# Kernel optimization log

Measured on AMD Instinct MI355X. Metric: run time of the kernel, lower is better.

The kernel has to match this reference:

```python
import jax, jax.numpy as jnp
import numpy as np

PATCH = 3
PAD = 1  # (patchsize-1)//2
PRETRAIN_DIM = 1024
TARGET_DIM = 1024
OUT_H, OUT_W = 224, 224


def _pool_matrix(L_in, L_out):
    """Matrix P s.t. x @ P == torch.adaptive_avg_pool1d(x, L_out)."""
    P = np.zeros((L_in, L_out), dtype=np.float32)
    for i in range(L_out):
        s = (i * L_in) // L_out
        e = -((-(i + 1) * L_in) // L_out)  # ceil
        P[s:e, i] = 1.0 / (e - s)
    return jnp.asarray(P)


def patchify(x):
    """[B,C,H,W] -> [B,H*W,C,3,3], matching Unfold(k=3,s=1,p=1) + reshape/permute."""
    B, C, H, W = x.shape
    xp = jnp.pad(x, ((0, 0), (0, 0), (PAD, PAD), (PAD, PAD)))
    # [B,C,3,3,H,W] with kernel offsets (ki,kj)
    cols = jnp.stack([
        jnp.stack([xp[:, :, i:i + H, j:j + W] for j in range(PATCH)], axis=3)
        for i in range(PATCH)], axis=2)
    return cols.transpose(0, 4, 5, 1, 2, 3).reshape(B, H * W, C, PATCH, PATCH)


def resize_bilinear(x, oh, ow):
    """Bilinear resize of last two dims, align_corners=False (torch semantics)."""
    H, W = x.shape[-2], x.shape[-1]

    def idx(L, O):
        src = (jnp.arange(O, dtype=jnp.float32) + 0.5) * (L / O) - 0.5
        src = jnp.clip(src, 0.0, L - 1)
        i0 = jnp.floor(src).astype(jnp.int32)
        i1 = jnp.minimum(i0 + 1, L - 1)
        return i0, i1, src - i0

    r0, r1, wr = idx(H, oh)
    c0, c1, wc = idx(W, ow)
    xr = x[..., r0, :] * (1.0 - wr)[:, None] + x[..., r1, :] * wr[:, None]
    return xr[..., c0] * (1.0 - wc) + xr[..., c1] * wc


def setup_inputs() -> dict:
    key = jax.random.key(0)
    k1, k2, k3 = jax.random.split(key, 3)
    return {
        "feat1": jax.random.normal(k1, (8, 512, 28, 28), dtype=jnp.float32),
        "feat2": jax.random.normal(k2, (8, 1024, 14, 14), dtype=jnp.float32),
        "memory": jax.random.normal(k3, (20000, 1024), dtype=jnp.float32),
    }


def reference(feat1, feat2, memory):
    B, C1, H1, W1 = feat1.shape
    _, C2, H2, W2 = feat2.shape
    N = H1 * W1  # reference patch grid

    # --- patchify (Unfold k=3 s=1 p=1) ---
    p1 = patchify(feat1)                      # [B, N, C1, 3, 3]
    p2 = patchify(feat2)                      # [B, H2*W2, C2, 3, 3]

    # --- multiscale bilinear resize of layer-2 patch grid to ref grid ---
    g = p2.reshape(B, H2, W2, C2, PATCH, PATCH).transpose(0, 3, 4, 5, 1, 2)  # [B,C2,3,3,H2,W2]
    g = resize_bilinear(g, H1, W1)                                           # [B,C2,3,3,H1,W1]
    p2 = g.transpose(0, 4, 5, 1, 2, 3).reshape(B, N, C2, PATCH, PATCH)

    # --- Preprocessing: adaptive_avg_pool1d over flattened patch -> pretrain dim ---
    f1 = p1.reshape(B * N, C1 * PATCH * PATCH) @ _pool_matrix(C1 * PATCH * PATCH, PRETRAIN_DIM)
    f2 = p2.reshape(B * N, C2 * PATCH * PATCH) @ _pool_matrix(C2 * PATCH * PATCH, PRETRAIN_DIM)

    # --- Aggregator: stack layers, adaptive pool to target dim ---
    stacked = jnp.stack([f1, f2], axis=1).reshape(B * N, 2 * PRETRAIN_DIM)
    feats = stacked @ _pool_matrix(2 * PRETRAIN_DIM, TARGET_DIM)  # [B*N, D]

    # --- kNN memory-bank scoring (k=1): min Euclidean distance ---
    d2 = (jnp.sum(feats * feats, axis=-1, keepdims=True)
          - 2.0 * feats @ memory.T
          + jnp.sum(memory * memory, axis=-1))  # [B*N, M]
    dist = jnp.sqrt(jnp.maximum(d2, 0.0))
    patch_scores = jnp.min(dist, axis=1)       # [B*N]

    # --- unpatch + score + raw segmentation map ---
    ps = patch_scores.reshape(B, N)
    image_scores = jnp.max(ps, axis=1)                           # [B]
    raw_maps = resize_bilinear(ps.reshape(B, H1, W1), OUT_H, OUT_W)  # [B,224,224]
    return image_scores, raw_maps
```

## Files before the change

kernel.cpp:

```cpp
#include <hip/hip_runtime.h>
#include <hip/hip_bf16.h>
#include <math.h>

#define BQ 8
#define C1N 512
#define N1 784
#define C2N 1024
#define M2 196
#define NROWS 6272
#define MEMN 20000
#define MEMNP 20096
#define DIMK 1024
#define NKB 32
#define KTB 4096
#define OUTHW 50176
#define NTILEA 49
#define NTILEB 157
#define NWG (NTILEB * NTILEA)

typedef unsigned char u8;
typedef long long i64v;

typedef __attribute__((ext_vector_type(4))) float f32x4;

static __device__ __forceinline__ unsigned int f2ord(float f) {
  unsigned int b = __float_as_uint(f);
  return (b & 0x80000000u) ? ~b : (b | 0x80000000u);
}
static __device__ __forceinline__ float ord2f(unsigned int u) {
  unsigned int b = (u & 0x80000000u) ? (u ^ 0x80000000u) : ~u;
  return __uint_as_float(b);
}

static __device__ __forceinline__ int pack4_fp8(float a, float b, float c, float d) {
  int lo = __builtin_amdgcn_cvt_pk_fp8_f32(a, b, 0, false);
  return __builtin_amdgcn_cvt_pk_fp8_f32(c, d, lo, true);
}
static __device__ __forceinline__ float sumsq4_fp8(int w) {
  float f0 = __builtin_amdgcn_cvt_f32_fp8(w, 0);
  float f1 = __builtin_amdgcn_cvt_f32_fp8(w, 1);
  float f2 = __builtin_amdgcn_cvt_f32_fp8(w, 2);
  float f3 = __builtin_amdgcn_cvt_f32_fp8(w, 3);
  return f0 * f0 + f1 * f1 + f2 * f2 + f3 * f3;
}

static __device__ __forceinline__ void gload16(const void* g, void* l) {
  __builtin_amdgcn_global_load_lds((const __attribute__((address_space(1))) void*)g,
                                   (__attribute__((address_space(3))) void*)l, 16, 0, 0);
}

static __device__ __forceinline__ size_t tiled_idx(int grow, int k) {
  int tile = grow >> 7, row = grow & 127;
  int kb = k >> 5, c = (k >> 3) & 3, e = k & 7;
  return (((size_t)(tile * NKB + kb) * 4 + c) * 128 + row) * 8 + e;
}

static __device__ __forceinline__ float f1val(const float* __restrict__ x, int b, unsigned L) {
  unsigned h = L % 28u; unsigned t = L / 28u;
  unsigned ki = t % 3u; t /= 3u;
  unsigned c = t % 512u; t /= 512u;
  unsigned w = t % 28u; unsigned kj = t / 28u;
  unsigned y = h + ki - 1u;
  unsigned xx = w + kj - 1u;
  if (y >= 28u || xx >= 28u) return 0.f;
  return x[(((size_t)b * 512u + c) * 28u + y) * 28u + xx];
}
static __device__ __forceinline__ float f2val(const float* __restrict__ x, int b, unsigned L) {
  unsigned h = L % 14u; unsigned t = L / 14u;
  unsigned ki = t % 3u; t /= 3u;
  unsigned c = t % 1024u; t /= 1024u;
  unsigned w = t % 14u; unsigned kj = t / 14u;
  unsigned y = h + ki - 1u;
  unsigned xx = w + kj - 1u;
  if (y >= 14u || xx >= 14u) return 0.f;
  return x[(((size_t)b * 1024u + c) * 14u + y) * 14u + xx];
}

__global__ __launch_bounds__(256) void feat_a_fp8(const float* __restrict__ feat1,
                                                  u8* __restrict__ At) {
  int id = blockIdx.x * 256 + threadIdx.x;
  if (id >= BQ * 64 * N1) return;
  int n = id % N1; int t = id / N1;
  int jc = t % 64; int b = t / 64;
  float v[8];
#pragma unroll
  for (int e = 0; e < 8; ++e) {
    int j = jc * 8 + e;
    unsigned L0 = 9u * (unsigned)(512 * n + j);
    float s = 0.f;
#pragma unroll
    for (int u = 0; u < 9; ++u) s += f1val(feat1, b, L0 + u);
    s += f1val(feat1, b, L0 + 4u);
    v[e] = s * 0.1f;
  }
  int w0 = pack4_fp8(v[0], v[1], v[2], v[3]);
  int w1 = pack4_fp8(v[4], v[5], v[6], v[7]);
  *(int2*)&At[tiled_idx(b * N1 + n, jc * 8)] = make_int2(w0, w1);
}

__global__ __launch_bounds__(256) void feat_b_stage1(const float* __restrict__ feat2,
                                                     float* __restrict__ H2all) {
  int b = blockIdx.x / M2;
  int n2 = blockIdx.x % M2;
  for (int i = threadIdx.x; i < 512; i += 256) {
    unsigned L0 = 18u * (unsigned)(512 * n2 + i);
    float s = 0.f;
#pragma unroll
    for (int u = 0; u < 18; ++u) s += f2val(feat2, b, L0 + u);
    H2all[((size_t)b * M2 + n2) * 512 + i] = s * (1.0f / 18.0f);
  }
}

__global__ __launch_bounds__(256) void feat_b_stage2_fp8(const float* __restrict__ H2all,
                                                         u8* __restrict__ At) {
  int id = blockIdx.x * 256 + threadIdx.x;
  if (id >= BQ * 64 * N1) return;
  int n = id % N1; int t = id / N1;
  int ic = t % 64; int b = t / 64;
  int y = n / 28, x = n % 28;
  float sy = 0.5f * (float)y - 0.25f;
  sy = fminf(fmaxf(sy, 0.f), 13.f);
  int y0 = (int)sy, y1 = min(y0 + 1, 13);
  float wy = sy - (float)y0;
  float sx = 0.5f * (float)x - 0.25f;
  sx = fminf(fmaxf(sx, 0.f), 13.f);
  int x0 = (int)sx, x1 = min(x0 + 1, 13);
  float wx = sx - (float)x0;
  float w00 = (1.f - wy) * (1.f - wx), w10 = wy * (1.f - wx);
  float w01 = (1.f - wy) * wx, w11 = wy * wx;
  const float* h00 = H2all + ((size_t)b * M2 + y0 * 14 + x0) * 512 + ic * 8;
  const float* h10 = H2all + ((size_t)b * M2 + y1 * 14 + x0) * 512 + ic * 8;
  const float* h01 = H2all + ((size_t)b * M2 + y0 * 14 + x1) * 512 + ic * 8;
  const float* h11 = H2all + ((size_t)b * M2 + y1 * 14 + x1) * 512 + ic * 8;
  float v[8];
#pragma unroll
  for (int e = 0; e < 8; ++e)
    v[e] = w00 * h00[e] + w10 * h10[e] + w01 * h01[e] + w11 * h11[e];
  int w0 = pack4_fp8(v[0], v[1], v[2], v[3]);
  int w1 = pack4_fp8(v[4], v[5], v[6], v[7]);
  *(int2*)&At[tiled_idx(b * N1 + n, 512 + ic * 8)] = make_int2(w0, w1);
}

__global__ __launch_bounds__(256) void memconv_fp8(const float* __restrict__ mem,
                                                   u8* __restrict__ Bt) {
  int gid = blockIdx.x * 256 + threadIdx.x;
  if (gid >= NTILEB * NKB * 512) return;
  int tile = gid >> 14;
  int within = gid & 16383;
  int kb = within >> 9;
  int u = within & 511;
  int c = u >> 7, row = u & 127;
  int n = tile * 128 + row;
  int k0 = kb * 32 + c * 8;
  int w0 = 0, w1 = 0;
  if (n < MEMN) {
    const float* src = mem + (size_t)n * DIMK + k0;
    float4 a = *(const float4*)src;
    float4 b = *(const float4*)(src + 4);
    w0 = pack4_fp8(a.x, a.y, a.z, a.w);
    w1 = pack4_fp8(b.x, b.y, b.z, b.w);
  }
  *(int2*)&Bt[(size_t)gid * 8] = make_int2(w0, w1);
}

__global__ __launch_bounds__(256) void fnorm_fp8(const u8* __restrict__ At,
                                                 float* __restrict__ fnorm) {
  int row = blockIdx.x * 4 + (threadIdx.x >> 6);
  int lane = threadIdx.x & 63;
  float s = 0.f;
#pragma unroll
  for (int qq = 0; qq < 2; ++qq) {
    int kc = lane * 2 + qq;
    int2 d = *(const int2*)&At[tiled_idx(row, kc * 8)];
    s += sumsq4_fp8(d.x);
    s += sumsq4_fp8(d.y);
  }
#pragma unroll
  for (int off = 32; off; off >>= 1) s += __shfl_down(s, off, 64);
  if (lane == 0) fnorm[row] = s;
}

__global__ __launch_bounds__(256) void mnorm_fp8(const float* __restrict__ memory,
                                                 float* __restrict__ mnorm) {
  __shared__ float red[4];
  const int row = blockIdx.x;
  const float4 v = *(const float4*)&memory[(size_t)row * DIMK + threadIdx.x * 4];
  int p0 = __builtin_amdgcn_cvt_pk_fp8_f32(v.x, v.y, 0, false);
  int p1 = __builtin_amdgcn_cvt_pk_fp8_f32(v.z, v.w, 0, false);
  float q0 = __builtin_amdgcn_cvt_f32_fp8(p0, 0);
  float q1 = __builtin_amdgcn_cvt_f32_fp8(p0, 1);
  float q2 = __builtin_amdgcn_cvt_f32_fp8(p1, 0);
  float q3 = __builtin_amdgcn_cvt_f32_fp8(p1, 1);
  float s = q0 * q0 + q1 * q1 + q2 * q2 + q3 * q3;
#pragma unroll
  for (int off = 32; off; off >>= 1) s += __shfl_down(s, off, 64);
  if ((threadIdx.x & 63) == 0) red[threadIdx.x >> 6] = s;
  __syncthreads();
  if (threadIdx.x == 0) mnorm[row] = red[0] + red[1] + red[2] + red[3];
}

__global__ __launch_bounds__(256, 4) void dist_min_mfma(const u8* __restrict__ At,
                                                        const u8* __restrict__ Bt,
                                                        const float* __restrict__ mnorm,
                                                        unsigned int* __restrict__ minu) {
  __shared__ __align__(16) u8 LAs[3][4096];
  __shared__ __align__(16) u8 LBs[3][4096];
  const int t = threadIdx.x;
  const int wave = t >> 6, lane = t & 63;

  int lid = blockIdx.x;
  const int q = NWG / 8, r = NWG % 8;
  int xcd = lid & 7, pos = lid >> 3;
  int wgid = (xcd < r ? xcd * (q + 1) : r * (q + 1) + (xcd - r) * q) + pos;
  int g = wgid / (NTILEB * 7), rem = wgid % (NTILEB * 7);
  int bx = rem / 7;
  int by = g * 7 + rem % 7;
  const int row0 = by * 128, col0 = bx * 128;

  f32x4 acc[4][4];
#pragma unroll
  for (int i = 0; i < 4; ++i)
#pragma unroll
    for (int j = 0; j < 4; ++j) acc[i][j] = (f32x4){0.f, 0.f, 0.f, 0.f};

  const int wr = (wave >> 1) * 64, wc = (wave & 1) * 64;
  const int frow = lane & 15, fc = lane >> 4;
  const int aoff = fc * 1024 + (wr + frow) * 8;
  const int boff = fc * 1024 + (wc + frow) * 8;
  const int soff = wave * 1024 + lane * 16;

  const u8* aG = At + (size_t)by * (NKB * KTB) + soff;
  const u8* bG = Bt + (size_t)bx * (NKB * KTB) + soff;

#define STAGE(buf)                            \
  do {                                        \
    gload16(aG, &LAs[buf][wave * 1024]);      \
    gload16(bG, &LBs[buf][wave * 1024]);      \
    aG += KTB; bG += KTB;                     \
  } while (0)

#define COMPUTE(buf)                                                                         \
  do {                                                                                       \
    i64v a[4], b[4];                                                                         \
    _Pragma("unroll") for (int mi = 0; mi < 4; ++mi)                                         \
        a[mi] = *(const i64v*)&LAs[buf][aoff + mi * 128];                                    \
    _Pragma("unroll") for (int ni = 0; ni < 4; ++ni)                                         \
        b[ni] = *(const i64v*)&LBs[buf][boff + ni * 128];                                    \
    __builtin_amdgcn_s_setprio(1);                                                           \
    _Pragma("unroll") for (int mi = 0; mi < 4; ++mi)                                         \
      _Pragma("unroll") for (int ni = 0; ni < 4; ++ni)                                       \
          acc[mi][ni] = __builtin_amdgcn_mfma_f32_16x16x32_fp8_fp8(a[mi], b[ni],             \
                                                                   acc[mi][ni], 0, 0, 0);    \
    __builtin_amdgcn_s_setprio(0);                                                           \
  } while (0)

#define WAITBAR(n)                                        \
  do {                                                    \
    asm volatile("s_waitcnt vmcnt(" #n ")" ::: "memory"); \
    __builtin_amdgcn_s_barrier();                         \
  } while (0)

  STAGE(0);
  STAGE(1);
  WAITBAR(2);

#pragma unroll 1
  for (int i = 0; i < 10; ++i) {
    STAGE(2); COMPUTE(0); WAITBAR(2);
    STAGE(0); COMPUTE(1); WAITBAR(2);
    STAGE(1); COMPUTE(2); WAITBAR(2);
  }
  COMPUTE(0);
  WAITBAR(0);
  COMPUTE(1);
#undef STAGE
#undef COMPUTE
#undef WAITBAR

  float cmn[4];
#pragma unroll
  for (int ni = 0; ni < 4; ++ni) {
    int gn = col0 + wc + ni * 16 + frow;
    cmn[ni] = (gn < MEMN) ? mnorm[gn] : INFINITY;
  }
#pragma unroll
  for (int mi = 0; mi < 4; ++mi) {
#pragma unroll
    for (int rr = 0; rr < 4; ++rr) {
      float v = INFINITY;
#pragma unroll
      for (int ni = 0; ni < 4; ++ni)
        v = fminf(v, fmaf(-2.f, acc[mi][ni][rr], cmn[ni]));
#pragma unroll
      for (int off = 1; off < 16; off <<= 1)
        v = fminf(v, __shfl_xor(v, off, 64));
      if (frow == 0) {
        int grow = row0 + wr + mi * 16 + (lane >> 4) * 4 + rr;
        atomicMin(&minu[grow], f2ord(v));
      }
    }
  }
}


__global__ __launch_bounds__(256) void scores_kernel(const float* __restrict__ fnorm,
                                                     const unsigned int* __restrict__ minu,
                                                     float* __restrict__ scores) {
  int row = blockIdx.x * 256 + threadIdx.x;
  if (row >= NROWS) return;
  float d2 = fnorm[row] + ord2f(minu[row]);
  scores[row] = sqrtf(fmaxf(d2, 0.f));
}

__global__ __launch_bounds__(256) void image_max_kernel(const float* __restrict__ scores,
                                                        float* __restrict__ out) {
  __shared__ float red[4];
  const int b = blockIdx.x;
  float m = -INFINITY;
  for (int n = threadIdx.x; n < N1; n += 256) m = fmaxf(m, scores[b * N1 + n]);
#pragma unroll
  for (int off = 32; off; off >>= 1) m = fmaxf(m, __shfl_down(m, off, 64));
  if ((threadIdx.x & 63) == 0) red[threadIdx.x >> 6] = m;
  __syncthreads();
  if (threadIdx.x == 0) out[b] = fmaxf(fmaxf(red[0], red[1]), fmaxf(red[2], red[3]));
}

__global__ __launch_bounds__(256) void upsample_kernel(const float* __restrict__ scores,
                                                       float* __restrict__ out) {
  int o = blockIdx.x * 256 + threadIdx.x;
  if (o >= BQ * OUTHW) return;
  int b = o / OUTHW, rem = o % OUTHW;
  int oy = rem / 224, ox = rem % 224;
  float sy = ((float)oy + 0.5f) * 0.125f - 0.5f;
  sy = fminf(fmaxf(sy, 0.f), 27.f);
  int y0 = (int)sy, y1 = min(y0 + 1, 27);
  float wy = sy - (float)y0;
  float sx = ((float)ox + 0.5f) * 0.125f - 0.5f;
  sx = fminf(fmaxf(sx, 0.f), 27.f);
  int x0 = (int)sx, x1 = min(x0 + 1, 27);
  float wx = sx - (float)x0;
  const float* s = scores + b * N1;
  float v0 = s[y0 * 28 + x0] * (1.f - wy) + s[y1 * 28 + x0] * wy;
  float v1 = s[y0 * 28 + x1] * (1.f - wy) + s[y1 * 28 + x1] * wy;
  out[BQ + o] = v0 * (1.f - wx) + v1 * wx;
}

extern "C" void kernel_launch(void* const* d_in, const int* in_sizes, int n_in,
                              void* d_out, int out_size, void* d_ws, size_t ws_size,
                              hipStream_t stream) {
  const float* feat1 = (const float*)d_in[0];
  const float* feat2 = (const float*)d_in[1];
  const float* memory = (const float*)d_in[2];
  float* out = (float*)d_out;

  char* ws = (char*)d_ws;
  size_t off = 0;
  auto wsalloc = [&](size_t bytes) {
    void* p = ws + off;
    off += (bytes + 255) & ~(size_t)255;
    return p;
  };

  u8* At = (u8*)wsalloc((size_t)NTILEA * NKB * KTB);
  u8* Bt = (u8*)wsalloc((size_t)NTILEB * NKB * KTB);
  float* mnorm = (float*)wsalloc((size_t)MEMN * 4);
  float* fnorm = (float*)wsalloc((size_t)NROWS * 4);
  unsigned int* minu = (unsigned int*)wsalloc((size_t)NROWS * 4);
  float* scores = (float*)wsalloc((size_t)NROWS * 4);
  float* H2all = (float*)Bt;

  feat_a_fp8<<<(BQ * 64 * N1) / 256, 256, 0, stream>>>(feat1, At);
  feat_b_stage1<<<BQ * M2, 256, 0, stream>>>(feat2, H2all);
  feat_b_stage2_fp8<<<(BQ * 64 * N1) / 256, 256, 0, stream>>>(H2all, At);
  memconv_fp8<<<(NTILEB * NKB * 512) / 256, 256, 0, stream>>>(memory, Bt);
  fnorm_fp8<<<NROWS / 4, 256, 0, stream>>>(At, fnorm);
  mnorm_fp8<<<MEMN, 256, 0, stream>>>(memory, mnorm);
  hipMemsetAsync(minu, 0xFF, (size_t)NROWS * 4, stream);

  dist_min_mfma<<<NWG, 256, 0, stream>>>(At, Bt, mnorm, minu);

  scores_kernel<<<(NROWS + 255) / 256, 256, 0, stream>>>(fnorm, minu, scores);
  image_max_kernel<<<BQ, 256, 0, stream>>>(scores, out);
  upsample_kernel<<<(BQ * OUTHW + 255) / 256, 256, 0, stream>>>(scores, out);
}
```

Before: 364.7 us.

## Switch distance GEMM to 16x16x128 scaled FP8 MFMA with swizzled K-slabs

Replaces the 16x16x32 fp8 MFMA with the gfx950 mfma_scale 16x16x128 f8f6f4 instruction using unit scales, so each instruction covers four times the K depth. The packed A/B layouts change to 128-wide K slabs of 16-byte chunks with an XOR swizzle meant to avoid LDS bank conflicts. The pipeline goes from triple-buffered 4KB stages to double-buffered 16KB stages with full vmcnt(0) waits. Occupancy drops to 2 workgroups per CU because of the larger LDS footprint. The producer kernels and fnorm are rewritten to write and read the new layout.

Result: faster. 346.3 us (-5.0%).

```diff
diff --git a/kernel.cpp b/kernel.cpp
--- a/kernel.cpp
+++ b/kernel.cpp
@@ -11,16 +11,15 @@
 #define MEMN 20000
 #define MEMNP 20096
 #define DIMK 1024
-#define NKB 32
-#define KTB 4096
+#define NSLAB 8
+#define SLB 16384
 #define OUTHW 50176
 #define NTILEA 49
 #define NTILEB 157
 #define NWG (NTILEB * NTILEA)
 
 typedef unsigned char u8;
-typedef long long i64v;
-
+typedef __attribute__((ext_vector_type(8))) int i32x8;
 typedef __attribute__((ext_vector_type(4))) float f32x4;
 
 static __device__ __forceinline__ unsigned int f2ord(float f) {
@@ -49,10 +48,12 @@
                                    (__attribute__((address_space(3))) void*)l, 16, 0, 0);
 }
 
-static __device__ __forceinline__ size_t tiled_idx(int grow, int k) {
+static __device__ __forceinline__ size_t chunk_addr(int grow, int k) {
   int tile = grow >> 7, row = grow & 127;
-  int kb = k >> 5, c = (k >> 3) & 3, e = k & 7;
-  return (((size_t)(tile * NKB + kb) * 4 + c) * 128 + row) * 8 + e;
+  int kb = k >> 7;
+  int c = ((k >> 5) & 3) * 256 + row * 2 + ((k >> 4) & 1);
+  int p = c ^ ((c >> 3) & 7);
+  return ((size_t)(tile * NSLAB + kb) * 1024 + p) * 16;
 }
 
 static __device__ __forceinline__ float f1val(const float* __restrict__ x, int b, unsigned L) {
@@ -95,7 +96,8 @@
   }
   int w0 = pack4_fp8(v[0], v[1], v[2], v[3]);
   int w1 = pack4_fp8(v[4], v[5], v[6], v[7]);
-  *(int2*)&At[tiled_idx(b * N1 + n, jc * 8)] = make_int2(w0, w1);
+  int k0 = jc * 8;
+  *(int2*)&At[chunk_addr(b * N1 + n, k0) + (k0 & 15)] = make_int2(w0, w1);
 }
 
 __global__ __launch_bounds__(256) void feat_b_stage1(const float* __restrict__ feat2,
@@ -138,43 +140,42 @@
     v[e] = w00 * h00[e] + w10 * h10[e] + w01 * h01[e] + w11 * h11[e];
   int w0 = pack4_fp8(v[0], v[1], v[2], v[3]);
   int w1 = pack4_fp8(v[4], v[5], v[6], v[7]);
-  *(int2*)&At[tiled_idx(b * N1 + n, 512 + ic * 8)] = make_int2(w0, w1);
+  int k0 = 512 + ic * 8;
+  *(int2*)&At[chunk_addr(b * N1 + n, k0) + (k0 & 15)] = make_int2(w0, w1);
 }
 
 __global__ __launch_bounds__(256) void memconv_fp8(const float* __restrict__ mem,
                                                    u8* __restrict__ Bt) {
   int gid = blockIdx.x * 256 + threadIdx.x;
-  if (gid >= NTILEB * NKB * 512) return;
-  int tile = gid >> 14;
-  int within = gid & 16383;
-  int kb = within >> 9;
-  int u = within & 511;
-  int c = u >> 7, row = u & 127;
+  if (gid >= NTILEB * NSLAB * 1024) return;
+  int p = gid & 1023;
+  int kb = (gid >> 10) & 7;
+  int tile = gid >> 13;
+  int c = p ^ ((p >> 3) & 7);
+  int fc = c >> 8, row = (c >> 1) & 127, h = c & 1;
   int n = tile * 128 + row;
-  int k0 = kb * 32 + c * 8;
-  int w0 = 0, w1 = 0;
+  int k0 = kb * 128 + fc * 32 + h * 16;
+  int4 o = make_int4(0, 0, 0, 0);
   if (n < MEMN) {
     const float* src = mem + (size_t)n * DIMK + k0;
     float4 a = *(const float4*)src;
     float4 b = *(const float4*)(src + 4);
-    w0 = pack4_fp8(a.x, a.y, a.z, a.w);
-    w1 = pack4_fp8(b.x, b.y, b.z, b.w);
-  }
-  *(int2*)&Bt[(size_t)gid * 8] = make_int2(w0, w1);
+    float4 cc = *(const float4*)(src + 8);
+    float4 d = *(const float4*)(src + 12);
+    o.x = pack4_fp8(a.x, a.y, a.z, a.w);
+    o.y = pack4_fp8(b.x, b.y, b.z, b.w);
+    o.z = pack4_fp8(cc.x, cc.y, cc.z, cc.w);
+    o.w = pack4_fp8(d.x, d.y, d.z, d.w);
+  }
+  *(int4*)&Bt[(size_t)gid * 16] = o;
 }
 
 __global__ __launch_bounds__(256) void fnorm_fp8(const u8* __restrict__ At,
                                                  float* __restrict__ fnorm) {
   int row = blockIdx.x * 4 + (threadIdx.x >> 6);
   int lane = threadIdx.x & 63;
-  float s = 0.f;
-#pragma unroll
-  for (int qq = 0; qq < 2; ++qq) {
-    int kc = lane * 2 + qq;
-    int2 d = *(const int2*)&At[tiled_idx(row, kc * 8)];
-    s += sumsq4_fp8(d.x);
-    s += sumsq4_fp8(d.y);
-  }
+  int4 d = *(const int4*)&At[chunk_addr(row, lane * 16)];
+  float s = sumsq4_fp8(d.x) + sumsq4_fp8(d.y) + sumsq4_fp8(d.z) + sumsq4_fp8(d.w);
 #pragma unroll
   for (int off = 32; off; off >>= 1) s += __shfl_down(s, off, 64);
   if (lane == 0) fnorm[row] = s;
@@ -199,12 +200,12 @@
   if (threadIdx.x == 0) mnorm[row] = red[0] + red[1] + red[2] + red[3];
 }
 
-__global__ __launch_bounds__(256, 4) void dist_min_mfma(const u8* __restrict__ At,
+__global__ __launch_bounds__(256, 2) void dist_min_mfma(const u8* __restrict__ At,
                                                         const u8* __restrict__ Bt,
                                                         const float* __restrict__ mnorm,
                                                         unsigned int* __restrict__ minu) {
-  __shared__ __align__(16) u8 LAs[3][4096];
-  __shared__ __align__(16) u8 LBs[3][4096];
+  __shared__ __align__(16) u8 LAs[2][SLB];
+  __shared__ __align__(16) u8 LBs[2][SLB];
   const int t = threadIdx.x;
   const int wave = t >> 6, lane = t & 63;
 
@@ -225,57 +226,73 @@
 
   const int wr = (wave >> 1) * 64, wc = (wave & 1) * 64;
   const int frow = lane & 15, fc = lane >> 4;
-  const int aoff = fc * 1024 + (wr + frow) * 8;
-  const int boff = fc * 1024 + (wc + frow) * 8;
-  const int soff = wave * 1024 + lane * 16;
-
-  const u8* aG = At + (size_t)by * (NKB * KTB) + soff;
-  const u8* bG = Bt + (size_t)bx * (NKB * KTB) + soff;
-
-#define STAGE(buf)                            \
-  do {                                        \
-    gload16(aG, &LAs[buf][wave * 1024]);      \
-    gload16(bG, &LBs[buf][wave * 1024]);      \
-    aG += KTB; bG += KTB;                     \
+
+  int aCh[4][2], bCh[4][2];
+#pragma unroll
+  for (int mi = 0; mi < 4; ++mi) {
+    int R = wr + mi * 16 + frow;
+    int C = wc + mi * 16 + frow;
+#pragma unroll
+    for (int h = 0; h < 2; ++h) {
+      int ca = fc * 256 + R * 2 + h;
+      aCh[mi][h] = (ca ^ ((ca >> 3) & 7)) * 16;
+      int cb = fc * 256 + C * 2 + h;
+      bCh[mi][h] = (cb ^ ((cb >> 3) & 7)) * 16;
+    }
+  }
+
+  const int sdst = wave * 1024;
+  const u8* aG = At + (size_t)by * (NSLAB * SLB) + wave * 1024 + lane * 16;
+  const u8* bG = Bt + (size_t)bx * (NSLAB * SLB) + wave * 1024 + lane * 16;
+
+#define STAGE(S)                                          \
+  do {                                                    \
+    _Pragma("unroll") for (int rr = 0; rr < 4; ++rr)      \
+        gload16(aG + rr * 4096, &LAs[S][rr * 4096 + sdst]); \
+    _Pragma("unroll") for (int rr = 0; rr < 4; ++rr)      \
+        gload16(bG + rr * 4096, &LBs[S][rr * 4096 + sdst]); \
+    aG += SLB; bG += SLB;                                 \
   } while (0)
 
-#define COMPUTE(buf)                                                                         \
+#define COMPUTE(S)                                                                           \
   do {                                                                                       \
-    i64v a[4], b[4];                                                                         \
-    _Pragma("unroll") for (int mi = 0; mi < 4; ++mi)                                         \
-        a[mi] = *(const i64v*)&LAs[buf][aoff + mi * 128];                                    \
-    _Pragma("unroll") for (int ni = 0; ni < 4; ++ni)                                         \
-        b[ni] = *(const i64v*)&LBs[buf][boff + ni * 128];                                    \
+    i32x8 a[4], b[4];                                                                        \
+    _Pragma("unroll") for (int mi = 0; mi < 4; ++mi) {                                       \
+      int4 lo = *(const int4*)&LAs[S][aCh[mi][0]];                                           \
+      int4 hi = *(const int4*)&LAs[S][aCh[mi][1]];                                           \
+      a[mi] = (i32x8){lo.x, lo.y, lo.z, lo.w, hi.x, hi.y, hi.z, hi.w};                       \
+    }                                                                                        \
+    _Pragma("unroll") for (int ni = 0; ni < 4; ++ni) {                                       \
+      int4 lo = *(const int4*)&LBs[S][bCh[ni][0]];                                           \
+      int4 hi = *(const int4*)&LBs[S][bCh[ni][1]];                                           \
+      b[ni] = (i32x8){lo.x, lo.y, lo.z, lo.w, hi.x, hi.y, hi.z, hi.w};                       \
+    }                                                                                        \
     __builtin_amdgcn_s_setprio(1);                                                           \
     _Pragma("unroll") for (int mi = 0; mi < 4; ++mi)                                         \
       _Pragma("unroll") for (int ni = 0; ni < 4; ++ni)                                       \
-          acc[mi][ni] = __builtin_amdgcn_mfma_f32_16x16x32_fp8_fp8(a[mi], b[ni],             \
-                                                                   acc[mi][ni], 0, 0, 0);    \
+          acc[mi][ni] = __builtin_amdgcn_mfma_scale_f32_16x16x128_f8f6f4(                    \
+              a[mi], b[ni], acc[mi][ni], 0, 0, 0, 0x7F7F7F7F, 0, 0x7F7F7F7F);                \
     __builtin_amdgcn_s_setprio(0);                                                           \
   } while (0)
 
-#define WAITBAR(n)                                        \
-  do {                                                    \
-    asm volatile("s_waitcnt vmcnt(" #n ")" ::: "memory"); \
-    __builtin_amdgcn_s_barrier();                         \
-  } while (0)
+#define VMW0 asm volatile("s_waitcnt vmcnt(0)" ::: "memory")
+#define SBAR __builtin_amdgcn_s_barrier()
 
   STAGE(0);
-  STAGE(1);
-  WAITBAR(2);
+  VMW0;
+  SBAR;
 
 #pragma unroll 1
-  for (int i = 0; i < 10; ++i) {
-    STAGE(2); COMPUTE(0); WAITBAR(2);
-    STAGE(0); COMPUTE(1); WAITBAR(2);
-    STAGE(1); COMPUTE(2); WAITBAR(2);
-  }
-  COMPUTE(0);
-  WAITBAR(0);
+  for (int i = 0; i < 3; ++i) {
+    STAGE(1); COMPUTE(0); VMW0; SBAR;
+    STAGE(0); COMPUTE(1); VMW0; SBAR;
+  }
+  STAGE(1); COMPUTE(0); VMW0; SBAR;
   COMPUTE(1);
 #undef STAGE
 #undef COMPUTE
-#undef WAITBAR
+#undef VMW0
+#undef SBAR
 
   float cmn[4];
 #pragma unroll
@@ -361,8 +378,8 @@
     return p;
   };
 
-  u8* At = (u8*)wsalloc((size_t)NTILEA * NKB * KTB);
-  u8* Bt = (u8*)wsalloc((size_t)NTILEB * NKB * KTB);
+  u8* At = (u8*)wsalloc((size_t)NTILEA * NSLAB * SLB);
+  u8* Bt = (u8*)wsalloc((size_t)NTILEB * NSLAB * SLB);
   float* mnorm = (float*)wsalloc((size_t)MEMN * 4);
   float* fnorm = (float*)wsalloc((size_t)NROWS * 4);
   unsigned int* minu = (unsigned int*)wsalloc((size_t)NROWS * 4);
@@ -372,10 +389,10 @@
   feat_a_fp8<<<(BQ * 64 * N1) / 256, 256, 0, stream>>>(feat1, At);
   feat_b_stage1<<<BQ * M2, 256, 0, stream>>>(feat2, H2all);
   feat_b_stage2_fp8<<<(BQ * 64 * N1) / 256, 256, 0, stream>>>(H2all, At);
-  memconv_fp8<<<(NTILEB * NKB * 512) / 256, 256, 0, stream>>>(memory, Bt);
+  memconv_fp8<<<(NTILEB * NSLAB * 1024) / 256, 256, 0, stream>>>(memory, Bt);
   fnorm_fp8<<<NROWS / 4, 256, 0, stream>>>(At, fnorm);
   mnorm_fp8<<<MEMN, 256, 0, stream>>>(memory, mnorm);
-  hipMemsetAsync(minu, 0xFF, (size_t)NROWS * 4, stream);
+  (void)hipMemsetAsync(minu, 0xFF, (size_t)NROWS * 4, stream);
 
   dist_min_mfma<<<NWG, 256, 0, stream>>>(At, Bt, mnorm, minu);
 
```
